# Kernel tuning notes

Measured on AMD Instinct MI355X. Metric: run time of the kernel, lower is better.

## Reference

```python
import jax, jax.numpy as jnp
import numpy as np

INPUT_SIZE, HIDDEN, OUTPUT, NUM_LAYERS = 128, 512, 64, 2
BATCH, SEQ = 64, 256


def setup_inputs() -> dict:
    key = jax.random.key(0)
    ks = jax.random.split(key, 4 * NUM_LAYERS + 3)
    s = 1.0 / np.sqrt(HIDDEN)  # PyTorch LSTM/Linear init scale
    inp = {"x": jax.random.normal(ks[0], (BATCH, SEQ, INPUT_SIZE), dtype=jnp.float32)}
    in_sz = INPUT_SIZE
    for l in range(NUM_LAYERS):
        k0, k1, k2, k3 = ks[1 + 4 * l:5 + 4 * l]
        inp[f"W_ih_{l}"] = jax.random.uniform(k0, (4 * HIDDEN, in_sz), minval=-s, maxval=s, dtype=jnp.float32)
        inp[f"W_hh_{l}"] = jax.random.uniform(k1, (4 * HIDDEN, HIDDEN), minval=-s, maxval=s, dtype=jnp.float32)
        inp[f"b_ih_{l}"] = jax.random.uniform(k2, (4 * HIDDEN,), minval=-s, maxval=s, dtype=jnp.float32)
        inp[f"b_hh_{l}"] = jax.random.uniform(k3, (4 * HIDDEN,), minval=-s, maxval=s, dtype=jnp.float32)
        in_sz = HIDDEN
    inp["W_fc"] = jax.random.uniform(ks[-2], (OUTPUT, HIDDEN), minval=-s, maxval=s, dtype=jnp.float32)
    inp["b_fc"] = jax.random.uniform(ks[-1], (OUTPUT,), minval=-s, maxval=s, dtype=jnp.float32)
    return inp


def _lstm_layer(x, W_ih, W_hh, b_ih, b_hh):
    # x: [B, T, D]. Precompute input-side gates for all timesteps (one big GEMM).
    B = x.shape[0]
    H = W_hh.shape[1]
    xg = jnp.einsum('btd,gd->btg', x, W_ih) + b_ih + b_hh  # [B, T, 4H]
    xg = jnp.swapaxes(xg, 0, 1)  # [T, B, 4H]

    def step(carry, xt):
        h, c = carry
        g = xt + h @ W_hh.T  # [B, 4H]; gate order i, f, g, o (PyTorch)
        i = jax.nn.sigmoid(g[:, 0 * H:1 * H])
        f = jax.nn.sigmoid(g[:, 1 * H:2 * H])
        gg = jnp.tanh(g[:, 2 * H:3 * H])
        o = jax.nn.sigmoid(g[:, 3 * H:4 * H])
        c = f * c + i * gg
        h = o * jnp.tanh(c)
        return (h, c), h

    h0 = jnp.zeros((B, H), dtype=x.dtype)
    (_, _), hs = jax.lax.scan(step, (h0, h0), xg)
    return jnp.swapaxes(hs, 0, 1)  # [B, T, H]


def reference(x, W_ih_0, W_hh_0, b_ih_0, b_hh_0, W_ih_1, W_hh_1, b_ih_1, b_hh_1, W_fc, b_fc):
    h = _lstm_layer(x, W_ih_0, W_hh_0, b_ih_0, b_hh_0)
    h = _lstm_layer(h, W_ih_1, W_hh_1, b_ih_1, b_hh_1)
    last = h[:, -1, :]  # [B, H]
    return last @ W_fc.T + b_fc  # [B, OUTPUT]
```

## Files before the change

### kernel.cpp

```cpp
#include <hip/hip_runtime.h>


#define NB    64
#define SEQL  256
#define INF   128
#define HID   512
#define OUTN  64
#define NWG   256
#define NT    256
#define NCNT  32
#define CADD  (NWG / NCNT)
#define PBOUND 4096

typedef __attribute__((ext_vector_type(8))) short  short8;
typedef __attribute__((ext_vector_type(4))) float  floatx4;
typedef unsigned short u16;
typedef unsigned long long u64;

#define TIE4(N, x0,x1,x2,x3)                                                \
  asm volatile("s_waitcnt vmcnt(" N ")" : "+v"(x0), "+v"(x1), "+v"(x2), "+v"(x3))
#define TIE2(N, x0,x1)                                                      \
  asm volatile("s_waitcnt vmcnt(" N ")" : "+v"(x0), "+v"(x1))

#define MFMA(ACC, A, B) \
  ACC = __builtin_amdgcn_mfma_f32_16x16x32_bf16((A), (B), ACC, 0, 0, 0)

__device__ __forceinline__ u16 f2bf(float f) {
  union { float f; unsigned u; } v; v.f = f;
  return (u16)((v.u + 0x7FFFu + ((v.u >> 16) & 1u)) >> 16);
}
__device__ __forceinline__ float bf2f(u16 s) {
  union { unsigned u; float f; } v; v.u = ((unsigned)s) << 16;
  return v.f;
}
__device__ __forceinline__ float sigf(float v) {
  return __builtin_amdgcn_rcpf(1.f + __expf(-v));
}
__device__ __forceinline__ float tanh_fast(float v) {
  float cv = fminf(fmaxf(v, -15.f), 15.f);
  float e = __expf(2.f * cv);
  return (e - 1.f) * __builtin_amdgcn_rcpf(e + 1.f);
}

__device__ __forceinline__ short8 ldh(const u16* p) {
  short8 d;
  asm volatile("global_load_dwordx4 %0, %1, off sc0 sc1" : "=v"(d) : "v"(p));
  return d;
}
__device__ __forceinline__ void st8c(u16* p, u64 v) {
  __hip_atomic_store((u64*)p, v, __ATOMIC_RELAXED, __HIP_MEMORY_SCOPE_AGENT);
}

__device__ __forceinline__ void wait_ge(const unsigned* f0, int thr0,
                                        const unsigned* f1, int thr1) {
  const int lane = threadIdx.x & 63;
  const unsigned* fp = nullptr;
  int thr = 0;
  if (lane < 16)      { fp = f0 + lane;        thr = thr0; }
  else if (lane < 32) { fp = f1 + (lane - 16); thr = thr1; }
  if (thr <= 0) fp = nullptr;
  for (int i = 0; i < PBOUND; ++i) {
    int v = 0x7fffffff;
    if (fp) v = (int)__hip_atomic_load(fp, __ATOMIC_RELAXED,
                                       __HIP_MEMORY_SCOPE_AGENT);
    if (__all(v >= thr)) break;
    if (i > 24) __builtin_amdgcn_s_sleep(1);
  }
  __builtin_amdgcn_sched_barrier(0);
  asm volatile("" ::: "memory");
}

__device__ __forceinline__ void grid_bar_once(unsigned* leaf, int w) {
  asm volatile("s_waitcnt vmcnt(0)" ::: "memory");
  __syncthreads();
  if (threadIdx.x == 0)
    __hip_atomic_fetch_add(&leaf[(w & (NCNT - 1)) * 32], 1u, __ATOMIC_RELAXED,
                           __HIP_MEMORY_SCOPE_AGENT);
  if (threadIdx.x < 64) {
    const int lane = threadIdx.x & 63;
    for (int i = 0; i < (1 << 16); ++i) {
      unsigned v = CADD;
      if (lane < NCNT)
        v = __hip_atomic_load(&leaf[lane * 32], __ATOMIC_RELAXED,
                              __HIP_MEMORY_SCOPE_AGENT);
      if (__all(v >= CADD)) break;
      __builtin_amdgcn_s_sleep(1);
    }
  }
  __syncthreads();
}

template <int KS, int KIN>
__device__ __forceinline__ void load_B(short8 (&Bf)[2][32],
                                       const float* __restrict__ Wih,
                                       const float* __restrict__ Whh,
                                       int li, int wv, int mrow, int quad) {
#pragma unroll
  for (int t2 = 0; t2 < 2; ++t2) {
    const int rowid = wv * 32 + t2 * 16 + mrow;
    const int r = (rowid & 3) * HID + 32 * li + (rowid >> 2);
    const float* wr = Wih + (size_t)r * KIN;
    const float* hr = Whh + (size_t)r * HID - KIN;
#pragma unroll
    for (int ks = 0; ks < KS; ++ks) {
      short8 v;
#pragma unroll
      for (int j = 0; j < 8; ++j) {
        const int k = 32 * ks + quad * 8 + j;
        v[j] = (short)f2bf(k < KIN ? wr[k] : hr[k]);
      }
      Bf[t2][ks] = v;
    }
  }
}

__global__ __launch_bounds__(NT, 1) void lstm_groups(
    const float* __restrict__ x,
    const float* __restrict__ Wih0, const float* __restrict__ Whh0,
    const float* __restrict__ bih0, const float* __restrict__ bhh0,
    const float* __restrict__ Wih1, const float* __restrict__ Whh1,
    const float* __restrict__ bih1, const float* __restrict__ bhh1,
    const float* __restrict__ Wfc,  const float* __restrict__ bfc,
    float* __restrict__ out,
    unsigned* __restrict__ leaf,
    unsigned* __restrict__ flag0, unsigned* __restrict__ flag1,
    u16* __restrict__ h0r, u16* __restrict__ h1r, u16* __restrict__ xg)
{
  const int w = blockIdx.x, tid = threadIdx.x;
  const int lane = tid & 63, wv = tid >> 6;
  const int quad = lane >> 4, mrow = lane & 15;
  const int g = w & 7, m = w >> 3;
  const bool isL1 = (m >= 16);
  const int  li   = isL1 ? m - 16 : m;

  __shared__ float g_lds[128][9];
  __shared__ u64   h_lds8[8][8];
  __shared__ float bias_lds[128];
  __shared__ float red[16][17];
  __shared__ short8 hA2[2][512];
  __shared__ short8 hB[512];
  char* hAc = (char*)hA2;
  char* hBc = (char*)hB;

#pragma unroll
  for (int i = 0; i < 8; ++i) {
    const int s = w * 8 + i, gs = s >> 8, ts = s & 255;
    u16* dst = xg + (size_t)(gs * 256 + ts) * 1024;
    const int b = tid >> 5, k0 = (tid & 31) * 4;
    const float* src = x + ((size_t)(8 * gs + b) * SEQL + ts) * INF + k0;
    union { u16 h[4]; u64 u; } pk;
#pragma unroll
    for (int j = 0; j < 4; ++j) pk.h[j] = f2bf(src[j]);
    st8c(dst + b * 128 + k0, pk.u);
  }

  short8 Bf[2][32];
  if (isL1) load_B<32, HID>(Bf, Wih1, Whh1, li, wv, mrow, quad);
  else      load_B<20, INF>(Bf, Wih0, Whh0, li, wv, mrow, quad);
  if (tid < 128) {
    const int r = (tid & 3) * HID + 32 * li + (tid >> 2);
    bias_lds[tid] = (isL1 ? bih1[r] + bhh1[r] : bih0[r] + bhh0[r]);
  }

  grid_bar_once(leaf, w);

  unsigned* flag0g = flag0 + g * 64;
  unsigned* flag1g = flag1 + g * 64;
  u16* h0g = h0r + (size_t)g * 32768;
  u16* h1g = h1r + (size_t)g * 32768;
  const u16* xgg = xg + (size_t)g * 256 * 1024;

  float cst = 0.f;
  const int ab = mrow & 7;
  const int koff = quad * 8;

  const int so0 = (tid * 16) ^ ((tid >> 6) << 4);
  const int so1 = ((tid + 256) * 16) ^ (((tid + 256) >> 6) << 4);

  if (isL1) {
    wait_ge(flag0g, 1, flag0g, 0);
    short8 s0 = ldh(h0g + tid * 8);
    short8 s1 = ldh(h0g + (tid + 256) * 8);
    TIE2("0", s0, s1);
    *(short8*)(hAc + so0) = s0;
    *(short8*)(hAc + so1) = s1;
    __syncthreads();
  }

  for (int t = 0; t < SEQL; ++t) {
    floatx4 a00 = {0,0,0,0}, a01 = {0,0,0,0}, a10 = {0,0,0,0}, a11 = {0,0,0,0};

    if (!isL1) {
      const u16* xa = xgg + (size_t)t * 1024 + ab * 128 + koff;
      short8 x0 = *(const short8*)(xa +  0);
      short8 x1 = *(const short8*)(xa + 32);
      short8 x2 = *(const short8*)(xa + 64);
      short8 x3 = *(const short8*)(xa + 96);
      MFMA(a00,x0,Bf[0][0]);  MFMA(a10,x0,Bf[1][0]);
      MFMA(a01,x1,Bf[0][1]);  MFMA(a11,x1,Bf[1][1]);
      MFMA(a00,x2,Bf[0][2]);  MFMA(a10,x2,Bf[1][2]);
      MFMA(a01,x3,Bf[0][3]);  MFMA(a11,x3,Bf[1][3]);

      wait_ge(flag0g, t, flag1g, t - 7);

      const u16* src = h0g + ((t + 7) & 7) * 4096;
      short8 s0 = ldh(src + tid * 8);
      short8 s1 = ldh(src + (tid + 256) * 8);
      TIE2("0", s0, s1);
      *(short8*)(hAc + so0) = s0;
      *(short8*)(hAc + so1) = s1;
      __syncthreads();

#pragma unroll
      for (int n = 0; n < 16; ++n) {
        const short8 fv = *(const short8*)(
            hAc + ((ab * 1024 + n * 64 + quad * 16) ^ (ab << 4)));
        if ((n & 1) == 0) { MFMA(a00, fv, Bf[0][4 + n]); MFMA(a10, fv, Bf[1][4 + n]); }
        else              { MFMA(a01, fv, Bf[0][4 + n]); MFMA(a11, fv, Bf[1][4 + n]); }
      }
    } else {
      const int thr0 = (t + 2 < 256) ? (t + 2) : 256;
      wait_ge(flag0g, thr0, flag1g, t);

      const u16* srcB = h1g + ((t + 7) & 7) * 4096;
      const u16* srcP = h0g + ((t + 1) & 7) * 4096;
      short8 sb0 = ldh(srcB + tid * 8);
      short8 sb1 = ldh(srcB + (tid + 256) * 8);
      short8 sp0 = ldh(srcP + tid * 8);
      short8 sp1 = ldh(srcP + (tid + 256) * 8);

      const char* hc = hAc + (t & 1) * 8192;
#pragma unroll
      for (int n = 0; n < 16; ++n) {
        const short8 fv = *(const short8*)(
            hc + ((ab * 1024 + n * 64 + quad * 16) ^ (ab << 4)));
        if ((n & 1) == 0) { MFMA(a00, fv, Bf[0][n]); MFMA(a10, fv, Bf[1][n]); }
        else              { MFMA(a01, fv, Bf[0][n]); MFMA(a11, fv, Bf[1][n]); }
      }

      TIE2("2", sb0, sb1);
      *(short8*)(hBc + so0) = sb0;
      *(short8*)(hBc + so1) = sb1;
      __syncthreads();

#pragma unroll
      for (int n = 0; n < 16; ++n) {
        const short8 fv = *(const short8*)(
            hBc + ((ab * 1024 + n * 64 + quad * 16) ^ (ab << 4)));
        if ((n & 1) == 0) { MFMA(a00, fv, Bf[0][16 + n]); MFMA(a10, fv, Bf[1][16 + n]); }
        else              { MFMA(a01, fv, Bf[0][16 + n]); MFMA(a11, fv, Bf[1][16 + n]); }
      }

      TIE2("0", sp0, sp1);
      *(short8*)(hAc + ((t + 1) & 1) * 8192 + so0) = sp0;
      *(short8*)(hAc + ((t + 1) & 1) * 8192 + so1) = sp1;
    }

    const floatx4 accA = a00 + a01, accB = a10 + a11;
    if (quad < 2) {
#pragma unroll
      for (int r = 0; r < 4; ++r) {
        g_lds[wv * 32 + mrow][quad * 4 + r]      = accA[r];
        g_lds[wv * 32 + 16 + mrow][quad * 4 + r] = accB[r];
      }
    }
    __syncthreads();

    {
      const int u = tid & 31, b = tid >> 5;
      const float gi = g_lds[u * 4 + 0][b] + bias_lds[u * 4 + 0];
      const float gf = g_lds[u * 4 + 1][b] + bias_lds[u * 4 + 1];
      const float gg = g_lds[u * 4 + 2][b] + bias_lds[u * 4 + 2];
      const float go = g_lds[u * 4 + 3][b] + bias_lds[u * 4 + 3];
      const float c = sigf(gf) * cst + sigf(gi) * tanh_fast(gg);
      cst = c;
      ((u16*)&h_lds8[b][0])[u] = f2bf(sigf(go) * tanh_fast(c));
    }
    __syncthreads();

    if (tid < 64) {
      const int b = tid >> 3, u8 = tid & 7;
      const u64 v = h_lds8[b][u8];
      u16* dst = (isL1 ? h1g : h0g) + (t & 7) * 4096 + b * 512 + li * 32 + u8 * 4;
      st8c(dst, v);
    }
    asm volatile("s_waitcnt vmcnt(0)" ::: "memory");
    if (tid == 0)
      __hip_atomic_store((isL1 ? flag1g : flag0g) + li, (unsigned)(t + 1),
                         __ATOMIC_RELAXED, __HIP_MEMORY_SCOPE_AGENT);
  }

  wait_ge(flag1g, 256, flag1g, 0);
  {
    const int bloc = m >> 2, oq = m & 3;
    const int ol = tid >> 4, ksub = tid & 15;
    const u16* hp = h1g + 7 * 4096 + bloc * 512 + ksub * 32;
    short8 v0 = ldh(hp),      v1 = ldh(hp + 8);
    short8 v2 = ldh(hp + 16), v3 = ldh(hp + 24);
    TIE4("0", v0, v1, v2, v3);
    const float* wr = Wfc + (size_t)(oq * 16 + ol) * HID + ksub * 32;
    float s = 0.f;
#pragma unroll
    for (int j = 0; j < 8; ++j) {
      s += bf2f((u16)v0[j]) * wr[j];
      s += bf2f((u16)v1[j]) * wr[8 + j];
      s += bf2f((u16)v2[j]) * wr[16 + j];
      s += bf2f((u16)v3[j]) * wr[24 + j];
    }
    red[ol][ksub] = s;
    __syncthreads();
    if (tid < 16) {
      float sum = 0.f;
#pragma unroll
      for (int j = 0; j < 16; ++j) sum += red[tid][j];
      out[(size_t)(8 * g + bloc) * OUTN + oq * 16 + tid] = sum + bfc[oq * 16 + tid];
    }
  }
}


extern "C" void kernel_launch(void* const* d_in, const int* in_sizes, int n_in,
                              void* d_out, int out_size, void* d_ws, size_t ws_size,
                              hipStream_t stream) {
  (void)in_sizes; (void)n_in; (void)out_size; (void)ws_size;

  char* ws = (char*)d_ws;
  unsigned* leaf  = (unsigned*)(ws + 256);
  unsigned* flag0 = (unsigned*)(ws + 8192);
  unsigned* flag1 = (unsigned*)(ws + 16384);
  u16* h0r = (u16*)(ws + 32768);
  u16* h1r = (u16*)(ws + 557056);
  u16* xg  = (u16*)(ws + 1081344);

  hipMemsetAsync(d_ws, 0, 1081344, stream);

  const float* x    = (const float*)d_in[0];
  const float* Wih0 = (const float*)d_in[1];
  const float* Whh0 = (const float*)d_in[2];
  const float* bih0 = (const float*)d_in[3];
  const float* bhh0 = (const float*)d_in[4];
  const float* Wih1 = (const float*)d_in[5];
  const float* Whh1 = (const float*)d_in[6];
  const float* bih1 = (const float*)d_in[7];
  const float* bhh1 = (const float*)d_in[8];
  const float* Wfc  = (const float*)d_in[9];
  const float* bfc  = (const float*)d_in[10];
  float* out = (float*)d_out;

  void* args[] = {
    (void*)&x,
    (void*)&Wih0, (void*)&Whh0, (void*)&bih0, (void*)&bhh0,
    (void*)&Wih1, (void*)&Whh1, (void*)&bih1, (void*)&bhh1,
    (void*)&Wfc,  (void*)&bfc,
    (void*)&out,
    (void*)&leaf, (void*)&flag0, (void*)&flag1,
    (void*)&h0r, (void*)&h1r, (void*)&xg
  };
  hipError_t err = hipLaunchCooperativeKernel((const void*)lstm_groups,
                                              dim3(NWG), dim3(NT), args, 0, stream);
  if (err != hipSuccess) {
    hipLaunchKernelGGL(lstm_groups, dim3(NWG), dim3(NT), 0, stream,
                       x, Wih0, Whh0, bih0, bhh0, Wih1, Whh1, bih1, bhh1,
                       Wfc, bfc, out, leaf, flag0, flag1, h0r, h1r, xg);
  }
}
```

Before: 1.070 ms.

## Compute LSTM cell in registers via lane shuffles with per-wave flags

Replaces the per-step LDS gate exchange and its two block barriers with an in-register 4x4 transpose via lane shuffles. Each wave now computes its own cell update, writes h directly to global memory, and publishes its own progress flag, so consumers poll 64 per-wave flags instead of 16 per-block ones. Bias is folded into the accumulator initialisation, and the LDS h buffers are double-buffered, allowing the layer-1 prefetch stores to move before the barrier. This removes intra-block synchronisation on the recurrent critical path, at the cost of more flag polling traffic and narrower 4-byte global stores.

```diff
diff --git a/kernel.cpp b/kernel.cpp
--- a/kernel.cpp
+++ b/kernel.cpp
@@ -10,7 +10,7 @@
 #define NT    256
 #define NCNT  32
 #define CADD  (NWG / NCNT)
-#define PBOUND 4096
+#define PBOUND 8192
 
 typedef __attribute__((ext_vector_type(8))) short  short8;
 typedef __attribute__((ext_vector_type(4))) float  floatx4;
@@ -50,20 +50,22 @@
 __device__ __forceinline__ void st8c(u16* p, u64 v) {
   __hip_atomic_store((u64*)p, v, __ATOMIC_RELAXED, __HIP_MEMORY_SCOPE_AGENT);
 }
-
-__device__ __forceinline__ void wait_ge(const unsigned* f0, int thr0,
-                                        const unsigned* f1, int thr1) {
+__device__ __forceinline__ void st4c(u16* p, unsigned v) {
+  __hip_atomic_store((unsigned*)p, v, __ATOMIC_RELAXED, __HIP_MEMORY_SCOPE_AGENT);
+}
+
+__device__ __forceinline__ void wait_ge64(const unsigned* f0, int thr0,
+                                          const unsigned* f1, int thr1) {
   const int lane = threadIdx.x & 63;
-  const unsigned* fp = nullptr;
-  int thr = 0;
-  if (lane < 16)      { fp = f0 + lane;        thr = thr0; }
-  else if (lane < 32) { fp = f1 + (lane - 16); thr = thr1; }
-  if (thr <= 0) fp = nullptr;
+  const unsigned* p0 = f0 + lane;
+  const unsigned* p1 = f1 + lane;
   for (int i = 0; i < PBOUND; ++i) {
-    int v = 0x7fffffff;
-    if (fp) v = (int)__hip_atomic_load(fp, __ATOMIC_RELAXED,
-                                       __HIP_MEMORY_SCOPE_AGENT);
-    if (__all(v >= thr)) break;
+    int a = 0x7fffffff, b = 0x7fffffff;
+    if (thr0 > 0) a = (int)__hip_atomic_load(p0, __ATOMIC_RELAXED,
+                                             __HIP_MEMORY_SCOPE_AGENT);
+    if (thr1 > 0) b = (int)__hip_atomic_load(p1, __ATOMIC_RELAXED,
+                                             __HIP_MEMORY_SCOPE_AGENT);
+    if (__all((a >= thr0) & (b >= thr1))) break;
     if (i > 24) __builtin_amdgcn_s_sleep(1);
   }
   __builtin_amdgcn_sched_barrier(0);
@@ -88,6 +90,26 @@
     }
   }
   __syncthreads();
+}
+
+__device__ __forceinline__ floatx4 xpose4(floatx4 v, int jb0, int jb1) {
+  floatx4 t;
+#pragma unroll
+  for (int r = 0; r < 4; ++r) t[r] = __shfl_xor(v[r], 1);
+  floatx4 u;
+  u[0] = jb0 ? t[1] : v[0];
+  u[1] = jb0 ? v[1] : t[0];
+  u[2] = jb0 ? t[3] : v[2];
+  u[3] = jb0 ? v[3] : t[2];
+  floatx4 s;
+#pragma unroll
+  for (int r = 0; r < 4; ++r) s[r] = __shfl_xor(u[r], 2);
+  floatx4 w_;
+  w_[0] = jb1 ? s[2] : u[0];
+  w_[1] = jb1 ? s[3] : u[1];
+  w_[2] = jb1 ? u[2] : s[0];
+  w_[3] = jb1 ? u[3] : s[1];
+  return w_;
 }
 
 template <int KS, int KIN>
@@ -133,14 +155,11 @@
   const bool isL1 = (m >= 16);
   const int  li   = isL1 ? m - 16 : m;
 
-  __shared__ float g_lds[128][9];
-  __shared__ u64   h_lds8[8][8];
-  __shared__ float bias_lds[128];
   __shared__ float red[16][17];
   __shared__ short8 hA2[2][512];
-  __shared__ short8 hB[512];
+  __shared__ short8 hB2[2][512];
   char* hAc = (char*)hA2;
-  char* hBc = (char*)hB;
+  char* hBc = (char*)hB2;
 
 #pragma unroll
   for (int i = 0; i < 8; ++i) {
@@ -157,9 +176,13 @@
   short8 Bf[2][32];
   if (isL1) load_B<32, HID>(Bf, Wih1, Whh1, li, wv, mrow, quad);
   else      load_B<20, INF>(Bf, Wih0, Whh0, li, wv, mrow, quad);
-  if (tid < 128) {
-    const int r = (tid & 3) * HID + 32 * li + (tid >> 2);
-    bias_lds[tid] = (isL1 ? bih1[r] + bhh1[r] : bih0[r] + bhh0[r]);
+  float bsA, bsB;
+  {
+    const int r0 = wv * 32 + mrow, r1 = r0 + 16;
+    const int ra = (r0 & 3) * HID + 32 * li + (r0 >> 2);
+    const int rb = (r1 & 3) * HID + 32 * li + (r1 >> 2);
+    bsA = isL1 ? (bih1[ra] + bhh1[ra]) : (bih0[ra] + bhh0[ra]);
+    bsB = isL1 ? (bih1[rb] + bhh1[rb]) : (bih0[rb] + bhh0[rb]);
   }
 
   grid_bar_once(leaf, w);
@@ -170,7 +193,10 @@
   u16* h1g = h1r + (size_t)g * 32768;
   const u16* xgg = xg + (size_t)g * 256 * 1024;
 
-  float cst = 0.f;
+  const int q4 = quad;
+  const int m4 = mrow >> 2, jg = mrow & 3;
+  const int jb0 = jg & 1, jb1 = (jg >> 1) & 1;
+  float cstA = 0.f, cstB = 0.f;
   const int ab = mrow & 7;
   const int koff = quad * 8;
 
@@ -178,7 +204,7 @@
   const int so1 = ((tid + 256) * 16) ^ (((tid + 256) >> 6) << 4);
 
   if (isL1) {
-    wait_ge(flag0g, 1, flag0g, 0);
+    wait_ge64(flag0g, 1, flag1g, 0);
     short8 s0 = ldh(h0g + tid * 8);
     short8 s1 = ldh(h0g + (tid + 256) * 8);
     TIE2("0", s0, s1);
@@ -188,7 +214,10 @@
   }
 
   for (int t = 0; t < SEQL; ++t) {
-    floatx4 a00 = {0,0,0,0}, a01 = {0,0,0,0}, a10 = {0,0,0,0}, a11 = {0,0,0,0};
+    floatx4 a00 = {bsA, bsA, bsA, bsA}, a01 = {0,0,0,0};
+    floatx4 a10 = {bsB, bsB, bsB, bsB}, a11 = {0,0,0,0};
+    const int pb = (t & 1) * 8192;
+    const int nb_ = ((t + 1) & 1) * 8192;
 
     if (!isL1) {
       const u16* xa = xgg + (size_t)t * 1024 + ab * 128 + koff;
@@ -201,26 +230,26 @@
       MFMA(a00,x2,Bf[0][2]);  MFMA(a10,x2,Bf[1][2]);
       MFMA(a01,x3,Bf[0][3]);  MFMA(a11,x3,Bf[1][3]);
 
-      wait_ge(flag0g, t, flag1g, t - 7);
+      wait_ge64(flag0g, t, flag1g, t - 7);
 
       const u16* src = h0g + ((t + 7) & 7) * 4096;
       short8 s0 = ldh(src + tid * 8);
       short8 s1 = ldh(src + (tid + 256) * 8);
       TIE2("0", s0, s1);
-      *(short8*)(hAc + so0) = s0;
-      *(short8*)(hAc + so1) = s1;
+      *(short8*)(hAc + pb + so0) = s0;
+      *(short8*)(hAc + pb + so1) = s1;
       __syncthreads();
 
 #pragma unroll
       for (int n = 0; n < 16; ++n) {
         const short8 fv = *(const short8*)(
-            hAc + ((ab * 1024 + n * 64 + quad * 16) ^ (ab << 4)));
+            hAc + pb + ((ab * 1024 + n * 64 + quad * 16) ^ (ab << 4)));
         if ((n & 1) == 0) { MFMA(a00, fv, Bf[0][4 + n]); MFMA(a10, fv, Bf[1][4 + n]); }
         else              { MFMA(a01, fv, Bf[0][4 + n]); MFMA(a11, fv, Bf[1][4 + n]); }
       }
     } else {
       const int thr0 = (t + 2 < 256) ? (t + 2) : 256;
-      wait_ge(flag0g, thr0, flag1g, t);
+      wait_ge64(flag0g, thr0, flag1g, t);
 
       const u16* srcB = h1g + ((t + 7) & 7) * 4096;
       const u16* srcP = h0g + ((t + 1) & 7) * 4096;
@@ -229,68 +258,57 @@
       short8 sp0 = ldh(srcP + tid * 8);
       short8 sp1 = ldh(srcP + (tid + 256) * 8);
 
-      const char* hc = hAc + (t & 1) * 8192;
 #pragma unroll
       for (int n = 0; n < 16; ++n) {
         const short8 fv = *(const short8*)(
-            hc + ((ab * 1024 + n * 64 + quad * 16) ^ (ab << 4)));
+            hAc + pb + ((ab * 1024 + n * 64 + quad * 16) ^ (ab << 4)));
         if ((n & 1) == 0) { MFMA(a00, fv, Bf[0][n]); MFMA(a10, fv, Bf[1][n]); }
         else              { MFMA(a01, fv, Bf[0][n]); MFMA(a11, fv, Bf[1][n]); }
       }
 
       TIE2("2", sb0, sb1);
-      *(short8*)(hBc + so0) = sb0;
-      *(short8*)(hBc + so1) = sb1;
+      *(short8*)(hBc + pb + so0) = sb0;
+      *(short8*)(hBc + pb + so1) = sb1;
+      TIE2("0", sp0, sp1);
+      *(short8*)(hAc + nb_ + so0) = sp0;
+      *(short8*)(hAc + nb_ + so1) = sp1;
       __syncthreads();
 
 #pragma unroll
       for (int n = 0; n < 16; ++n) {
         const short8 fv = *(const short8*)(
-            hBc + ((ab * 1024 + n * 64 + quad * 16) ^ (ab << 4)));
+            hBc + pb + ((ab * 1024 + n * 64 + quad * 16) ^ (ab << 4)));
         if ((n & 1) == 0) { MFMA(a00, fv, Bf[0][16 + n]); MFMA(a10, fv, Bf[1][16 + n]); }
         else              { MFMA(a01, fv, Bf[0][16 + n]); MFMA(a11, fv, Bf[1][16 + n]); }
       }
-
-      TIE2("0", sp0, sp1);
-      *(short8*)(hAc + ((t + 1) & 1) * 8192 + so0) = sp0;
-      *(short8*)(hAc + ((t + 1) & 1) * 8192 + so1) = sp1;
-    }
-
-    const floatx4 accA = a00 + a01, accB = a10 + a11;
-    if (quad < 2) {
-#pragma unroll
-      for (int r = 0; r < 4; ++r) {
-        g_lds[wv * 32 + mrow][quad * 4 + r]      = accA[r];
-        g_lds[wv * 32 + 16 + mrow][quad * 4 + r] = accB[r];
-      }
-    }
-    __syncthreads();
-
-    {
-      const int u = tid & 31, b = tid >> 5;
-      const float gi = g_lds[u * 4 + 0][b] + bias_lds[u * 4 + 0];
-      const float gf = g_lds[u * 4 + 1][b] + bias_lds[u * 4 + 1];
-      const float gg = g_lds[u * 4 + 2][b] + bias_lds[u * 4 + 2];
-      const float go = g_lds[u * 4 + 3][b] + bias_lds[u * 4 + 3];
-      const float c = sigf(gf) * cst + sigf(gi) * tanh_fast(gg);
-      cst = c;
-      ((u16*)&h_lds8[b][0])[u] = f2bf(sigf(go) * tanh_fast(c));
-    }
-    __syncthreads();
-
-    if (tid < 64) {
-      const int b = tid >> 3, u8 = tid & 7;
-      const u64 v = h_lds8[b][u8];
-      u16* dst = (isL1 ? h1g : h0g) + (t & 7) * 4096 + b * 512 + li * 32 + u8 * 4;
-      st8c(dst, v);
+    }
+
+    const floatx4 vA = a00 + a01, vB = a10 + a11;
+    if (lane < 32) {
+      const floatx4 gA = xpose4(vA, jb0, jb1);
+      const floatx4 gB = xpose4(vB, jb0, jb1);
+      const float cA = sigf(gA[1]) * cstA + sigf(gA[0]) * tanh_fast(gA[2]);
+      const float cB = sigf(gB[1]) * cstB + sigf(gB[0]) * tanh_fast(gB[2]);
+      cstA = cA; cstB = cB;
+      const unsigned hA16 = (unsigned)f2bf(sigf(gA[3]) * tanh_fast(cA));
+      const unsigned hB16 = (unsigned)f2bf(sigf(gB[3]) * tanh_fast(cB));
+      const unsigned pA = (unsigned)__shfl_xor((int)hA16, 4);
+      const unsigned pB = (unsigned)__shfl_xor((int)hB16, 4);
+      if ((m4 & 1) == 0) {
+        u16* base = (isL1 ? h1g : h0g) + (t & 7) * 4096 +
+                    (q4 * 4 + jg) * 512 + li * 32 + wv * 8 + m4;
+        st4c(base,     hA16 | (pA << 16));
+        st4c(base + 4, hB16 | (pB << 16));
+      }
     }
     asm volatile("s_waitcnt vmcnt(0)" ::: "memory");
-    if (tid == 0)
-      __hip_atomic_store((isL1 ? flag1g : flag0g) + li, (unsigned)(t + 1),
+    if (lane == 0)
+      __hip_atomic_store((isL1 ? flag1g : flag0g) + li * 4 + wv,
+                         (unsigned)(t + 1),
                          __ATOMIC_RELAXED, __HIP_MEMORY_SCOPE_AGENT);
   }
 
-  wait_ge(flag1g, 256, flag1g, 0);
+  wait_ge64(flag1g, 256, flag1g, 0);
   {
     const int bloc = m >> 2, oq = m & 3;
     const int ol = tid >> 4, ksub = tid & 15;
```

Result: slower. 2.708 ms (+153.0%).
